# Optimization experiments

Hardware: AMD Instinct MI355X
Metric: run time of the kernel (lower is better)

Reference implementation:

```python
import jax, jax.numpy as jnp
import numpy as np

N_TOKENS = 8192      # batch_seq (B*S)
HIDDEN = 2048        # hidden_size
N_EXPERTS = 64       # n_routed_experts
TOP_K = 8            # num_experts_per_tok
LBL_COEF = 0.01      # lbl_coef


def setup_inputs() -> dict:
    key = jax.random.key(0)
    k1, k2 = jax.random.split(key)
    return {
        "inputs_flat": jax.random.normal(k1, (N_TOKENS, HIDDEN), dtype=jnp.float32),
        "router_logits": jax.random.normal(k2, (N_TOKENS, N_EXPERTS), dtype=jnp.float32),
    }


def reference(inputs_flat, router_logits):
    # Router probabilities
    router_probs = jax.nn.softmax(router_logits, axis=-1)            # [N, E]

    # _route_local, TOP_K strategy: top-k then per-token weight normalization
    sel_w, sel_idx = jax.lax.top_k(router_probs, TOP_K)              # [N, k]
    sel_w = sel_w / sel_w.sum(-1, keepdims=True)

    # _replicate_and_sort_tokens: replicate each token k times, sort by expert id
    flat_idx = sel_idx.reshape(-1)                                   # [N*k]
    sorted_by_expert = jnp.argsort(flat_idx)                         # [N*k]
    replicated = jnp.repeat(inputs_flat, TOP_K, axis=0)              # [N*k, H]
    sorted_inputs = replicated[sorted_by_expert]                     # [N*k, H]
    sorted_w = sel_w.reshape(-1)[sorted_by_expert]                   # [N*k]
    weighted_sorted = sorted_inputs * sorted_w[:, None]              # [N*k, H]

    group_sizes = jnp.bincount(flat_idx, length=N_EXPERTS)           # [E]

    # STANDARD load-balancing loss: lbl * sum(f * p), f = loads*E/k, p = mean probs
    expert_loads = group_sizes.astype(jnp.float32) / flat_idx.shape[0]
    f = expert_loads * N_EXPERTS / TOP_K
    p = jnp.mean(router_probs, axis=0)
    lb_loss = LBL_COEF * jnp.sum(f * p)

    return weighted_sorted, group_sizes, lb_loss
```

## Files before the change

kernel.cpp:

```cpp
#include <hip/hip_runtime.h>
#include <math.h>

#define NTOK   8192
#define HID    2048
#define NEXP   64
#define TOPK   8
#define NFLAT  (NTOK * TOPK)
#define NB     256
#define OUT_GS_OFF  ((size_t)NFLAT * HID)
#define OUT_LB_OFF  (OUT_GS_OFF + NEXP)

typedef float f32x4 __attribute__((ext_vector_type(4)));

__global__ __launch_bounds__(256) void k_route(const float* __restrict__ logits,
                                               int*   __restrict__ e_rank,
                                               float* __restrict__ flat_w,
                                               int*   __restrict__ counts,
                                               float* __restrict__ probpart)
{
    __shared__ float sm[4][64];
    __shared__ unsigned mask[64];
    const int tid  = threadIdx.x;
    const int lane = tid & 63;
    const int wave = tid >> 6;
    if (tid < 64) mask[tid] = 0u;
    float acc = 0.f;
    __syncthreads();

    int   sel_i[8];
    float sel_v[8];
    float sum8s[8];

    #pragma unroll
    for (int it = 0; it < 8; ++it) {
        const int ti    = it * 4 + wave;
        const int token = blockIdx.x * 32 + ti;
        const float lg = logits[(size_t)token * NEXP + lane];
        float m = lg;
        #pragma unroll
        for (int off = 32; off; off >>= 1) m = fmaxf(m, __shfl_xor(m, off));
        const float ex = expf(lg - m);
        float s = ex;
        #pragma unroll
        for (int off = 32; off; off >>= 1) s += __shfl_xor(s, off);
        const float p = ex / s;
        acc += p;

        float v = p;
        float mysel_v = 0.f; int mysel_i = 0; float sum8 = 0.f;
        #pragma unroll
        for (int k = 0; k < TOPK; ++k) {
            float mv = v; int mi = lane;
            #pragma unroll
            for (int off = 32; off; off >>= 1) {
                const float ov = __shfl_xor(mv, off);
                const int   oi = __shfl_xor(mi, off);
                if (ov > mv || (ov == mv && oi < mi)) { mv = ov; mi = oi; }
            }
            if (lane == k)  { mysel_v = mv; mysel_i = mi; }
            if (lane == mi) v = -1.f;
            sum8 += mv;
        }
        sel_i[it] = mysel_i; sel_v[it] = mysel_v; sum8s[it] = sum8;
        if (lane < TOPK) atomicOr(&mask[mysel_i], 1u << ti);
    }

    sm[wave][lane] = acc;
    __syncthreads();

    if (tid < 64) {
        counts  [(size_t)tid * NB + blockIdx.x] = (int)__popc(mask[tid]);
        probpart[(size_t)tid * NB + blockIdx.x] =
            sm[0][tid] + sm[1][tid] + sm[2][tid] + sm[3][tid];
    }

    #pragma unroll
    for (int it = 0; it < 8; ++it) {
        const int ti    = it * 4 + wave;
        const int token = blockIdx.x * 32 + ti;
        if (lane < TOPK) {
            const int e    = sel_i[it];
            const int rank = (int)__popc(mask[e] & ((1u << ti) - 1u));
            e_rank[(size_t)token * TOPK + lane] = e | (rank << 8);
            flat_w[(size_t)token * TOPK + lane] = sel_v[it] / sum8s[it];
        }
    }
}

__global__ __launch_bounds__(256) void k_scan(const int*   __restrict__ counts,
                                              const float* __restrict__ probpart,
                                              int*   __restrict__ blockoff,
                                              float* __restrict__ out_gs,
                                              float* __restrict__ out_lb) {
    __shared__ int   part_c[64][4];
    __shared__ float part_p[64][4];
    __shared__ int   qoff[64][4];
    __shared__ int   totals[64];
    __shared__ float psums[64];
    __shared__ int   basesm[64];
    const int t = threadIdx.x;
    const int e = t >> 2;
    const int q = t & 3;

    int tot = 0; float ps = 0.f;
    const size_t base = (size_t)e * NB + q * 64;
    for (int b = 0; b < 64; b += 4) {
        const int4   c = *(const int4*)  &counts  [base + b];
        const float4 pp = *(const float4*)&probpart[base + b];
        tot += c.x + c.y + c.z + c.w;
        ps  += pp.x + pp.y + pp.z + pp.w;
    }
    part_c[e][q] = tot; part_p[e][q] = ps;
    __syncthreads();

    if (t < 64) {
        int c0 = part_c[t][0], c1 = part_c[t][1], c2 = part_c[t][2], c3 = part_c[t][3];
        qoff[t][0] = 0;
        qoff[t][1] = c0;
        qoff[t][2] = c0 + c1;
        qoff[t][3] = c0 + c1 + c2;
        totals[t]  = c0 + c1 + c2 + c3;
        psums[t]   = part_p[t][0] + part_p[t][1] + part_p[t][2] + part_p[t][3];
    }
    __syncthreads();

    if (t == 0) {
        int bacc = 0; float lb = 0.f;
        for (int i = 0; i < 64; ++i) {
            basesm[i] = bacc;
            bacc += totals[i];
            lb += ((float)totals[i] * (1.f / 8192.f)) * (psums[i] * (1.f / 8192.f));
        }
        *out_lb = 0.01f * lb;
    }
    __syncthreads();

    if (t < 64) out_gs[t] = (float)totals[t];

    int run = basesm[e] + qoff[e][q];
    for (int b = 0; b < 64; b += 4) {
        const int4 c = *(const int4*)&counts[base + b];
        int4 o;
        o.x = run;
        o.y = o.x + c.x;
        o.z = o.y + c.y;
        o.w = o.z + c.z;
        run = o.w + c.w;
        *(int4*)&blockoff[base + b] = o;
    }
}

__global__ __launch_bounds__(512) void k_copy(const float* __restrict__ x,
                                              const int*   __restrict__ e_rank,
                                              const float* __restrict__ flat_w,
                                              const int*   __restrict__ blockoff,
                                              float*       __restrict__ out) {
    const int token = blockIdx.x;
    __shared__ int   s_pos[8];
    __shared__ float s_w[8];
    const int t = threadIdx.x;
    if (t < TOPK) {
        const int er   = e_rank[(size_t)token * TOPK + t];
        const int e    = er & 0xff;
        const int rank = er >> 8;
        s_pos[t] = blockoff[(size_t)e * NB + (token >> 5)] + rank;
        s_w[t]   = flat_w[(size_t)token * TOPK + t];
    }
    __syncthreads();

    const f32x4* __restrict__ src = (const f32x4*)(x + (size_t)token * HID);
    const f32x4 a = src[t];

    #pragma unroll
    for (int k = 0; k < TOPK; ++k) {
        f32x4* dst = (f32x4*)(out + (size_t)s_pos[k] * HID);
        dst[t] = a * s_w[k];
    }
}

extern "C" void kernel_launch(void* const* d_in, const int* in_sizes, int n_in,
                              void* d_out, int out_size, void* d_ws, size_t ws_size,
                              hipStream_t stream) {
    const float* x      = (const float*)d_in[0];
    const float* logits = (const float*)d_in[1];
    float* out = (float*)d_out;

    char* ws = (char*)d_ws;
    int*   e_rank   = (int*)  (ws + 0);
    float* flat_w   = (float*)(ws + 262144);
    int*   counts   = (int*)  (ws + 524288);
    int*   blockoff = (int*)  (ws + 589824);
    float* probpart = (float*)(ws + 655360);

    k_route<<<NB, 256, 0, stream>>>(logits, e_rank, flat_w, counts, probpart);
    k_scan <<<1, 256, 0, stream>>>(counts, probpart, blockoff,
                                   out + OUT_GS_OFF, out + OUT_LB_OFF);
    k_copy <<<NTOK, 512, 0, stream>>>(x, e_rank, flat_w, blockoff, out);
}
```

Measured before the change: 177.3 us.

## Invert scatter into gather with per-row source table and nontemporal stores

Adds a kernel that builds an inverse map from each sorted output row to its source token and weight. The copy kernel then launches one block per output row, reads the source token row and writes its destination contiguously with nontemporal stores. Previously each token block scattered eight rows to destinations spread across the output. The intent is to make writes sequential and keep the 128 MB output from polluting cache. The cost is an extra kernel launch, an extra workspace buffer, and each input row being read eight times instead of once.

```diff
diff --git a/kernel.cpp b/kernel.cpp
--- a/kernel.cpp
+++ b/kernel.cpp
@@ -150,32 +150,34 @@
     }
 }
 
-__global__ __launch_bounds__(512) void k_copy(const float* __restrict__ x,
-                                              const int*   __restrict__ e_rank,
-                                              const float* __restrict__ flat_w,
-                                              const int*   __restrict__ blockoff,
+__global__ __launch_bounds__(256) void k_inv(const int*   __restrict__ e_rank,
+                                             const float* __restrict__ flat_w,
+                                             const int*   __restrict__ blockoff,
+                                             int2*        __restrict__ srcinfo) {
+    const int g = blockIdx.x * 256 + threadIdx.x;
+    const int er   = e_rank[g];
+    const int e    = er & 0xff;
+    const int rank = er >> 8;
+    const int r = blockoff[(size_t)e * NB + (g >> 8)] + rank;
+    int2 v;
+    v.x = g >> 3;
+    v.y = __float_as_int(flat_w[g]);
+    srcinfo[r] = v;
+}
+
+__global__ __launch_bounds__(256) void k_copy(const float* __restrict__ x,
+                                              const int2*  __restrict__ srcinfo,
                                               float*       __restrict__ out) {
-    const int token = blockIdx.x;
-    __shared__ int   s_pos[8];
-    __shared__ float s_w[8];
+    const int r = blockIdx.x;
+    const int2 si = srcinfo[r];
+    const float w = __int_as_float(si.y);
+    const f32x4* __restrict__ src = (const f32x4*)(x + (size_t)si.x * HID);
+    f32x4* __restrict__ dst = (f32x4*)(out + (size_t)r * HID);
     const int t = threadIdx.x;
-    if (t < TOPK) {
-        const int er   = e_rank[(size_t)token * TOPK + t];
-        const int e    = er & 0xff;
-        const int rank = er >> 8;
-        s_pos[t] = blockoff[(size_t)e * NB + (token >> 5)] + rank;
-        s_w[t]   = flat_w[(size_t)token * TOPK + t];
-    }
-    __syncthreads();
-
-    const f32x4* __restrict__ src = (const f32x4*)(x + (size_t)token * HID);
-    const f32x4 a = src[t];
-
-    #pragma unroll
-    for (int k = 0; k < TOPK; ++k) {
-        f32x4* dst = (f32x4*)(out + (size_t)s_pos[k] * HID);
-        dst[t] = a * s_w[k];
-    }
+    const f32x4 a = src[t] * w;
+    const f32x4 b = src[t + 256] * w;
+    __builtin_nontemporal_store(a, dst + t);
+    __builtin_nontemporal_store(b, dst + t + 256);
 }
 
 extern "C" void kernel_launch(void* const* d_in, const int* in_sizes, int n_in,
@@ -191,9 +193,11 @@
     int*   counts   = (int*)  (ws + 524288);
     int*   blockoff = (int*)  (ws + 589824);
     float* probpart = (float*)(ws + 655360);
+    int2*  srcinfo  = (int2*) (ws + 720896);
 
     k_route<<<NB, 256, 0, stream>>>(logits, e_rank, flat_w, counts, probpart);
     k_scan <<<1, 256, 0, stream>>>(counts, probpart, blockoff,
                                    out + OUT_GS_OFF, out + OUT_LB_OFF);
-    k_copy <<<NTOK, 512, 0, stream>>>(x, e_rank, flat_w, blockoff, out);
-}
+    k_inv  <<<NFLAT / 256, 256, 0, stream>>>(e_rank, flat_w, blockoff, srcinfo);
+    k_copy <<<NFLAT, 256, 0, stream>>>(x, srcinfo, out);
+}
```

Result: slower. 208.6 us (+17.7%).

## Persist copy kernel over multiple tokens with prefetch and nontemporal stores

Applied to the files above, without the earlier changes.

The scatter-copy kernel now runs a fixed grid of 2048 blocks of 256 threads, each processing four tokens. The next token's row, positions and weights are prefetched into double-buffered shared memory while the current token's eight weighted copies are written. Stores use nontemporal hints to avoid cache pollution from the large write-once output. This aims to hide load latency and reduce block launch overhead, at the cost of fewer blocks in flight and more registers per thread.

```diff
diff --git a/kernel.cpp b/kernel.cpp
--- a/kernel.cpp
+++ b/kernel.cpp
@@ -7,6 +7,7 @@
 #define TOPK   8
 #define NFLAT  (NTOK * TOPK)
 #define NB     256
+#define CGRID  2048
 #define OUT_GS_OFF  ((size_t)NFLAT * HID)
 #define OUT_LB_OFF  (OUT_GS_OFF + NEXP)
 
@@ -150,31 +151,51 @@
     }
 }
 
-__global__ __launch_bounds__(512) void k_copy(const float* __restrict__ x,
+__global__ __launch_bounds__(256) void k_copy(const float* __restrict__ x,
                                               const int*   __restrict__ e_rank,
                                               const float* __restrict__ flat_w,
                                               const int*   __restrict__ blockoff,
                                               float*       __restrict__ out) {
-    const int token = blockIdx.x;
-    __shared__ int   s_pos[8];
-    __shared__ float s_w[8];
+    __shared__ int   s_pos[2][8];
+    __shared__ float s_w[2][8];
     const int t = threadIdx.x;
+
+    int tok = blockIdx.x;
     if (t < TOPK) {
-        const int er   = e_rank[(size_t)token * TOPK + t];
-        const int e    = er & 0xff;
-        const int rank = er >> 8;
-        s_pos[t] = blockoff[(size_t)e * NB + (token >> 5)] + rank;
-        s_w[t]   = flat_w[(size_t)token * TOPK + t];
-    }
-    __syncthreads();
-
-    const f32x4* __restrict__ src = (const f32x4*)(x + (size_t)token * HID);
-    const f32x4 a = src[t];
+        const int er = e_rank[(size_t)tok * TOPK + t];
+        s_pos[0][t] = blockoff[(size_t)(er & 0xff) * NB + (tok >> 5)] + (er >> 8);
+        s_w[0][t]   = flat_w[(size_t)tok * TOPK + t];
+    }
+    const f32x4* __restrict__ src0 = (const f32x4*)(x + (size_t)tok * HID);
+    f32x4 a = src0[t];
+    f32x4 b = src0[t + 256];
+    __syncthreads();
 
     #pragma unroll
-    for (int k = 0; k < TOPK; ++k) {
-        f32x4* dst = (f32x4*)(out + (size_t)s_pos[k] * HID);
-        dst[t] = a * s_w[k];
+    for (int it = 0; it < 4; ++it) {
+        const int cur = it & 1;
+        const int nxt = cur ^ 1;
+        const int ntok = tok + CGRID;
+        f32x4 a1 = a, b1 = b;
+        if (it < 3) {
+            if (t < TOPK) {
+                const int er = e_rank[(size_t)ntok * TOPK + t];
+                s_pos[nxt][t] = blockoff[(size_t)(er & 0xff) * NB + (ntok >> 5)] + (er >> 8);
+                s_w[nxt][t]   = flat_w[(size_t)ntok * TOPK + t];
+            }
+            const f32x4* __restrict__ src1 = (const f32x4*)(x + (size_t)ntok * HID);
+            a1 = src1[t];
+            b1 = src1[t + 256];
+        }
+        #pragma unroll
+        for (int k = 0; k < TOPK; ++k) {
+            const float w = s_w[cur][k];
+            f32x4* dst = (f32x4*)(out + (size_t)s_pos[cur][k] * HID);
+            __builtin_nontemporal_store(a * w, dst + t);
+            __builtin_nontemporal_store(b * w, dst + t + 256);
+        }
+        __syncthreads();
+        a = a1; b = b1; tok = ntok;
     }
 }
 
@@ -195,5 +216,5 @@
     k_route<<<NB, 256, 0, stream>>>(logits, e_rank, flat_w, counts, probpart);
     k_scan <<<1, 256, 0, stream>>>(counts, probpart, blockoff,
                                    out + OUT_GS_OFF, out + OUT_LB_OFF);
-    k_copy <<<NTOK, 512, 0, stream>>>(x, e_rank, flat_w, blockoff, out);
-}
+    k_copy <<<CGRID, 256, 0, stream>>>(x, e_rank, flat_w, blockoff, out);
+}
```

After: 163.7 us. 1.08x faster.

## Fuse routing and scan via last-block pattern, widen route grid, nontemporal stores

Applied to the files above, without the earlier changes.

Routing now uses 1024 blocks of 8 tokens instead of 256 blocks of 32, so more CUs take part in the softmax and top-k phase. The separate scan kernel is folded into the route kernel: the last block to finish, detected with an atomic counter and threadfences, computes the prefix offsets, group sizes and load-balancing loss. This removes one kernel launch but adds a memset, an atomic, and a serial scan over four times as many per-block counts. The copy kernel also switches to nontemporal stores for the large scattered output.

```diff
diff --git a/kernel.cpp b/kernel.cpp
--- a/kernel.cpp
+++ b/kernel.cpp
@@ -6,20 +6,26 @@
 #define NEXP   64
 #define TOPK   8
 #define NFLAT  (NTOK * TOPK)
-#define NB     256
+#define NRB    1024
+#define TPB    8
 #define OUT_GS_OFF  ((size_t)NFLAT * HID)
 #define OUT_LB_OFF  (OUT_GS_OFF + NEXP)
 
 typedef float f32x4 __attribute__((ext_vector_type(4)));
 
-__global__ __launch_bounds__(256) void k_route(const float* __restrict__ logits,
-                                               int*   __restrict__ e_rank,
-                                               float* __restrict__ flat_w,
-                                               int*   __restrict__ counts,
-                                               float* __restrict__ probpart)
-{
+__global__ __launch_bounds__(256) void k_route_scan(
+        const float* __restrict__ logits,
+        int*      __restrict__ e_rank,
+        float*    __restrict__ flat_w,
+        int*      __restrict__ counts,
+        float*    __restrict__ probpart,
+        int*      __restrict__ blockoff,
+        unsigned* __restrict__ done,
+        float*    __restrict__ out_gs,
+        float*    __restrict__ out_lb) {
     __shared__ float sm[4][64];
     __shared__ unsigned mask[64];
+    __shared__ int amlast;
     const int tid  = threadIdx.x;
     const int lane = tid & 63;
     const int wave = tid >> 6;
@@ -27,14 +33,14 @@
     float acc = 0.f;
     __syncthreads();
 
-    int   sel_i[8];
-    float sel_v[8];
-    float sum8s[8];
+    int   sel_i[2];
+    float sel_v[2];
+    float sum8s[2];
 
     #pragma unroll
-    for (int it = 0; it < 8; ++it) {
+    for (int it = 0; it < 2; ++it) {
         const int ti    = it * 4 + wave;
-        const int token = blockIdx.x * 32 + ti;
+        const int token = blockIdx.x * TPB + ti;
         const float lg = logits[(size_t)token * NEXP + lane];
         float m = lg;
         #pragma unroll
@@ -69,15 +75,15 @@
     __syncthreads();
 
     if (tid < 64) {
-        counts  [(size_t)tid * NB + blockIdx.x] = (int)__popc(mask[tid]);
-        probpart[(size_t)tid * NB + blockIdx.x] =
+        counts  [(size_t)tid * NRB + blockIdx.x] = (int)__popc(mask[tid]);
+        probpart[(size_t)tid * NRB + blockIdx.x] =
             sm[0][tid] + sm[1][tid] + sm[2][tid] + sm[3][tid];
     }
 
     #pragma unroll
-    for (int it = 0; it < 8; ++it) {
+    for (int it = 0; it < 2; ++it) {
         const int ti    = it * 4 + wave;
-        const int token = blockIdx.x * 32 + ti;
+        const int token = blockIdx.x * TPB + ti;
         if (lane < TOPK) {
             const int e    = sel_i[it];
             const int rank = (int)__popc(mask[e] & ((1u << ti) - 1u));
@@ -85,27 +91,30 @@
             flat_w[(size_t)token * TOPK + lane] = sel_v[it] / sum8s[it];
         }
     }
-}
-
-__global__ __launch_bounds__(256) void k_scan(const int*   __restrict__ counts,
-                                              const float* __restrict__ probpart,
-                                              int*   __restrict__ blockoff,
-                                              float* __restrict__ out_gs,
-                                              float* __restrict__ out_lb) {
+
+    __threadfence();
+    __syncthreads();
+    if (tid == 0) {
+        const unsigned prev = atomicAdd(done, 1u);
+        amlast = (prev == NRB - 1) ? 1 : 0;
+    }
+    __syncthreads();
+    if (!amlast) return;
+    __threadfence();
+
     __shared__ int   part_c[64][4];
     __shared__ float part_p[64][4];
     __shared__ int   qoff[64][4];
     __shared__ int   totals[64];
     __shared__ float psums[64];
     __shared__ int   basesm[64];
-    const int t = threadIdx.x;
-    const int e = t >> 2;
-    const int q = t & 3;
+    const int e = tid >> 2;
+    const int q = tid & 3;
 
     int tot = 0; float ps = 0.f;
-    const size_t base = (size_t)e * NB + q * 64;
-    for (int b = 0; b < 64; b += 4) {
-        const int4   c = *(const int4*)  &counts  [base + b];
+    const size_t base = (size_t)e * NRB + q * (NRB / 4);
+    for (int b = 0; b < NRB / 4; b += 4) {
+        const int4   c  = *(const int4*)  &counts  [base + b];
         const float4 pp = *(const float4*)&probpart[base + b];
         tot += c.x + c.y + c.z + c.w;
         ps  += pp.x + pp.y + pp.z + pp.w;
@@ -113,18 +122,19 @@
     part_c[e][q] = tot; part_p[e][q] = ps;
     __syncthreads();
 
-    if (t < 64) {
-        int c0 = part_c[t][0], c1 = part_c[t][1], c2 = part_c[t][2], c3 = part_c[t][3];
-        qoff[t][0] = 0;
-        qoff[t][1] = c0;
-        qoff[t][2] = c0 + c1;
-        qoff[t][3] = c0 + c1 + c2;
-        totals[t]  = c0 + c1 + c2 + c3;
-        psums[t]   = part_p[t][0] + part_p[t][1] + part_p[t][2] + part_p[t][3];
-    }
-    __syncthreads();
-
-    if (t == 0) {
+    if (tid < 64) {
+        const int c0 = part_c[tid][0], c1 = part_c[tid][1],
+                  c2 = part_c[tid][2], c3 = part_c[tid][3];
+        qoff[tid][0] = 0;
+        qoff[tid][1] = c0;
+        qoff[tid][2] = c0 + c1;
+        qoff[tid][3] = c0 + c1 + c2;
+        totals[tid]  = c0 + c1 + c2 + c3;
+        psums[tid]   = part_p[tid][0] + part_p[tid][1] + part_p[tid][2] + part_p[tid][3];
+    }
+    __syncthreads();
+
+    if (tid == 0) {
         int bacc = 0; float lb = 0.f;
         for (int i = 0; i < 64; ++i) {
             basesm[i] = bacc;
@@ -135,10 +145,10 @@
     }
     __syncthreads();
 
-    if (t < 64) out_gs[t] = (float)totals[t];
+    if (tid < 64) out_gs[tid] = (float)totals[tid];
 
     int run = basesm[e] + qoff[e][q];
-    for (int b = 0; b < 64; b += 4) {
+    for (int b = 0; b < NRB / 4; b += 4) {
         const int4 c = *(const int4*)&counts[base + b];
         int4 o;
         o.x = run;
@@ -161,9 +171,7 @@
     const int t = threadIdx.x;
     if (t < TOPK) {
         const int er   = e_rank[(size_t)token * TOPK + t];
-        const int e    = er & 0xff;
-        const int rank = er >> 8;
-        s_pos[t] = blockoff[(size_t)e * NB + (token >> 5)] + rank;
+        s_pos[t] = blockoff[(size_t)(er & 0xff) * NRB + (token >> 3)] + (er >> 8);
         s_w[t]   = flat_w[(size_t)token * TOPK + t];
     }
     __syncthreads();
@@ -174,7 +182,7 @@
     #pragma unroll
     for (int k = 0; k < TOPK; ++k) {
         f32x4* dst = (f32x4*)(out + (size_t)s_pos[k] * HID);
-        dst[t] = a * s_w[k];
+        __builtin_nontemporal_store(a * s_w[k], dst + t);
     }
 }
 
@@ -186,14 +194,16 @@
     float* out = (float*)d_out;
 
     char* ws = (char*)d_ws;
-    int*   e_rank   = (int*)  (ws + 0);
-    float* flat_w   = (float*)(ws + 262144);
-    int*   counts   = (int*)  (ws + 524288);
-    int*   blockoff = (int*)  (ws + 589824);
-    float* probpart = (float*)(ws + 655360);
-
-    k_route<<<NB, 256, 0, stream>>>(logits, e_rank, flat_w, counts, probpart);
-    k_scan <<<1, 256, 0, stream>>>(counts, probpart, blockoff,
-                                   out + OUT_GS_OFF, out + OUT_LB_OFF);
-    k_copy <<<NTOK, 512, 0, stream>>>(x, e_rank, flat_w, blockoff, out);
+    int*      e_rank   = (int*)     (ws + 0);
+    float*    flat_w   = (float*)   (ws + 262144);
+    int*      counts   = (int*)     (ws + 524288);
+    int*      blockoff = (int*)     (ws + 786432);
+    float*    probpart = (float*)   (ws + 1048576);
+    unsigned* done     = (unsigned*)(ws + 1310720);
+
+    hipMemsetAsync(done, 0, sizeof(unsigned), stream);
+    k_route_scan<<<NRB, 256, 0, stream>>>(logits, e_rank, flat_w, counts,
+                                          probpart, blockoff, done,
+                                          out + OUT_GS_OFF, out + OUT_LB_OFF);
+    k_copy<<<NTOK, 512, 0, stream>>>(x, e_rank, flat_w, blockoff, out);
 }
```

After: 264.3 us. 1.49x slower.
